# Optimization experiments

Measured on AMD Instinct MI355X. Metric: run time of the kernel, lower is better.

The kernel has to match this reference:

```python
import jax, jax.numpy as jnp
import numpy as np

HEADS = 16
DIM_HEAD = 64


def setup_inputs() -> dict:
    key = jax.random.key(0)
    k1, k2, k3 = jax.random.split(key, 3)
    b, n, dim = 2, 2048, 1024
    x = jax.random.normal(k1, (b, n, dim), dtype=jnp.float32)
    W_qkv = jax.random.normal(k2, (dim, 6 * HEADS * DIM_HEAD), dtype=jnp.float32) * 0.02
    W_out = jax.random.normal(k3, (HEADS * DIM_HEAD, dim), dtype=jnp.float32) * 0.02
    return {"x": x, "W_qkv": W_qkv, "W_out": W_out}


def reference(x, W_qkv, W_out):
    b, n, _ = x.shape
    h, d = HEADS, DIM_HEAD
    scale = d ** -0.5

    # project and split into 6 head-wise tensors: (qkv h d) grouping order
    qkv = (x @ W_qkv).reshape(b, n, 6, h, d).transpose(2, 0, 3, 1, 4)  # [6,b,h,n,d]
    qu, ku, vu, qc, kc, vc = qkv
    qu_s = qu * scale
    qc_s = qc * scale

    idx = jnp.arange(n)
    future = idx[None, :] > idx[:, None]  # torch triu(1): True strictly above diag

    # term1: qc . vu, zeroed on future positions
    term1 = jnp.einsum('bhid,bhjd->bhij', qc_s, vu)
    term1 = jnp.where(future, 0.0, term1)

    # sigmoid lookahead attention, kept ONLY on strictly-future positions
    lookahead = jax.nn.sigmoid(jnp.einsum('bhid,bhjd->bhij', qu_s, ku))
    lookahead = jnp.where(future, lookahead, 0.0)

    # Su[i,k] = sum_j term1[i,j] * lookahead[k,j]
    Su = jnp.einsum('bhij,bhkj->bhik', term1, lookahead)
    Sc = jnp.einsum('bhid,bhjd->bhij', qc_s, kc)

    scores = Sc - jax.nn.silu(Su)
    neg = -jnp.finfo(scores.dtype).max
    scores = jnp.where(future, neg, scores)

    attn = jax.nn.softmax(scores, axis=-1)
    out = jnp.einsum('bhij,bhjd->bhid', attn, vc)  # [b,h,n,d]

    out = out.transpose(0, 2, 1, 3).reshape(b, n, h * d)
    return out @ W_out
```

## Files before the change

### kernel.cpp

```cpp
#include <hip/hip_runtime.h>
#include <hip/hip_bf16.h>
#include <stdint.h>


typedef unsigned short u16;
typedef __attribute__((ext_vector_type(8))) short s8v;
typedef __attribute__((ext_vector_type(4))) float f4v;

__device__ __forceinline__ u16 f2bf(float f) {
  union { float f; unsigned u; } v; v.f = f;
  unsigned r = v.u + 0x7FFFu + ((v.u >> 16) & 1u);
  return (u16)(r >> 16);
}
__device__ __forceinline__ float bf2f(u16 u) {
  union { unsigned u; float f; } v; v.u = ((unsigned)u) << 16; return v.f;
}

typedef __attribute__((address_space(1))) const void* gas_t;
typedef __attribute__((address_space(3))) void* las_t;
__device__ __forceinline__ void gld16(const void* g, void* l) {
  __builtin_amdgcn_global_load_lds((gas_t)g, (las_t)l, 16, 0, 0);
}

__device__ __forceinline__ void zero_acc(f4v acc[4][4]) {
  f4v z = {0.f, 0.f, 0.f, 0.f};
#pragma unroll
  for (int m = 0; m < 4; ++m)
#pragma unroll
    for (int n = 0; n < 4; ++n) acc[m][n] = z;
}


__global__ void convert_x_kernel(const float* __restrict__ in, u16* __restrict__ out) {
  int i = (blockIdx.x * 256 + threadIdx.x) * 4;
  float4 v = *(const float4*)(&in[i]);
  out[i + 0] = f2bf(v.x);
  out[i + 1] = f2bf(v.y);
  out[i + 2] = f2bf(v.z);
  out[i + 3] = f2bf(v.w);
}

__global__ void transpose_convert_kernel(const float* __restrict__ in, u16* __restrict__ out,
                                         int R, int C) {
  __shared__ float tile[32][33];
  int c0 = blockIdx.x * 32, r0 = blockIdx.y * 32;
  for (int rr = threadIdx.y; rr < 32; rr += 8)
    tile[rr][threadIdx.x] = in[(size_t)(r0 + rr) * C + (c0 + threadIdx.x)];
  __syncthreads();
  for (int cc = threadIdx.y; cc < 32; cc += 8)
    out[(size_t)(c0 + cc) * R + (r0 + threadIdx.x)] = f2bf(tile[threadIdx.x][cc]);
}


__global__ __launch_bounds__(256, 2) void gemm_qkv_kernel(
    const u16* __restrict__ xb, const u16* __restrict__ wqkvT,
    u16* __restrict__ quS, u16* __restrict__ ku, u16* __restrict__ vu,
    u16* __restrict__ qcS, u16* __restrict__ kc, u16* __restrict__ vcN) {
  __shared__ u16 sA[2][8192];
  __shared__ u16 sB[2][8192];
  int bm = blockIdx.x, bn = blockIdx.y;
  int tid = threadIdx.x, lane = tid & 63, w = tid >> 6, wm = w >> 1, wn = w & 1;
  int g = lane >> 4, l15 = lane & 15;
  const int sz = (l15 & 7) << 3;
  const int bo = tid * 16;

  const u16* Ab = xb + (size_t)(bm * 128) * 1024;
  const u16* Bb = wqkvT + (size_t)(bn * 128) * 1024;

  auto stg = [&](const u16* base, int ks, u16* dst) {
#pragma unroll
    for (int it = 0; it < 4; ++it) {
      int o = bo + it * 4096;
      int row = o >> 7, lo = o & 127;
      gld16(base + (size_t)row * 1024 + ks * 64 + ((lo ^ ((row & 7) << 4)) >> 1),
            (char*)dst + o);
    }
  };

  f4v acc[4][4];
  zero_acc(acc);
  stg(Ab, 0, sA[0]);
  stg(Bb, 0, sB[0]);
  stg(Ab, 1, sA[1]);
  stg(Bb, 1, sB[1]);

  for (int ks = 0; ks < 16; ++ks) {
    int buf = ks & 1;
    if (ks < 15)
      asm volatile("s_waitcnt vmcnt(8)" ::: "memory");
    else
      asm volatile("s_waitcnt vmcnt(0)" ::: "memory");
    __builtin_amdgcn_sched_barrier(0);
    __builtin_amdgcn_s_barrier();
    __builtin_amdgcn_sched_barrier(0);
#pragma unroll
    for (int kk = 0; kk < 2; ++kk) {
      int c2 = kk * 32 + g * 8;
      s8v a[4], b[4];
#pragma unroll
      for (int m = 0; m < 4; ++m)
        a[m] = *(const s8v*)(&sA[buf][(wm * 64 + m * 16 + l15) * 64 + (c2 ^ sz)]);
#pragma unroll
      for (int n = 0; n < 4; ++n)
        b[n] = *(const s8v*)(&sB[buf][(wn * 64 + n * 16 + l15) * 64 + (c2 ^ sz)]);
#pragma unroll
      for (int m = 0; m < 4; ++m)
#pragma unroll
        for (int n = 0; n < 4; ++n)
          acc[m][n] = __builtin_amdgcn_mfma_f32_16x16x32_bf16(a[m], b[n], acc[m][n], 0, 0, 0);
    }
    __builtin_amdgcn_s_barrier();
    if (ks + 2 < 16) {
      stg(Ab, ks + 2, sA[buf]);
      stg(Bb, ks + 2, sB[buf]);
    }
  }

  int s = bn >> 3;
  int b = bm >> 4;
  int nn0 = (bm & 15) * 128;
  int hh0 = (bn & 7) * 2;
  float scale = (s == 0 || s == 3) ? 0.125f : 1.f;
  u16* obase;
  switch (s) {
    case 0: obase = quS; break;
    case 1: obase = ku; break;
    case 2: obase = vu; break;
    case 3: obase = qcS; break;
    case 4: obase = kc; break;
    default: obase = vcN; break;
  }
  u16* sE = (u16*)sA;
#pragma unroll
  for (int pass = 0; pass < 2; ++pass) {
    __syncthreads();
    if (wn == pass) {
#pragma unroll
      for (int m = 0; m < 4; ++m)
#pragma unroll
        for (int n = 0; n < 4; ++n)
#pragma unroll
          for (int j = 0; j < 4; ++j) {
            int lrow = wm * 64 + m * 16 + g * 4 + j;
            int d = n * 16 + l15;
            sE[lrow * 64 + d] = f2bf(acc[m][n][j] * scale);
          }
    }
    __syncthreads();
    int bh = (b << 4) + hh0 + pass;
    u16* dst = obase + ((size_t)bh * 2048 + nn0) * 64;
    for (int it = 0; it < 4; ++it) {
      int e = (tid + it * 256) * 8;
      *(uint4*)(dst + e) = *(const uint4*)(&sE[e]);
    }
  }
}


__global__ __launch_bounds__(256) void transpose_v_kernel(const u16* __restrict__ vcN,
                                                          u16* __restrict__ vcT) {
  __shared__ u16 t[64][72];
  int nt = blockIdx.x, bh = blockIdx.y;
  const u16* src = vcN + ((size_t)bh * 2048 + nt * 64) * 64;
  int tid = threadIdx.x;
  for (int i = tid; i < 512; i += 256) {
    int r = i >> 3, cseg = i & 7;
    *(uint4*)(&t[r][cseg * 8]) = *(const uint4*)(src + r * 64 + cseg * 8);
  }
  __syncthreads();
  u16* dst = vcT + (size_t)bh * 64 * 2048 + nt * 64;
  for (int i = tid; i < 512; i += 256) {
    int d = i >> 3, nseg = i & 7;
    u16 tmp[8];
#pragma unroll
    for (int e = 0; e < 8; ++e) tmp[e] = t[nseg * 8 + e][d];
    *(uint4*)(dst + (size_t)d * 2048 + nseg * 8) = *(uint4*)tmp;
  }
}


__global__ __launch_bounds__(256, 2) void tl_kernel(
    const u16* __restrict__ qcS, const u16* __restrict__ vu,
    const u16* __restrict__ quS, const u16* __restrict__ ku,
    u16* __restrict__ term1p, u16* __restrict__ lookp, int c0) {
  __shared__ u16 S[32768];
  int t = blockIdx.x, lb = blockIdx.y, bh = c0 + lb;
  int I = 0;
  while ((I + 1) * (I + 2) / 2 <= t) ++I;
  int K = t - I * (I + 1) / 2;
  int tid = threadIdx.x, lane = tid & 63, w = tid >> 6, wm = w >> 1, wn = w & 1;
  int g = lane >> 4, l15 = lane & 15;
  const int sz = (l15 & 7) << 3;
  const int bo = tid * 16;

  auto stg = [&](const u16* base, int rt, u16* dst) {
#pragma unroll
    for (int it = 0; it < 4; ++it) {
      int o = bo + it * 4096;
      int row = o >> 7, lo = o & 127;
      gld16(base + ((size_t)bh * 2048 + rt * 128 + row) * 64 + ((lo ^ ((row & 7) << 4)) >> 1),
            (char*)dst + o);
    }
  };
  stg(qcS, I, S);
  stg(vu, K, S + 8192);
  stg(quS, K, S + 16384);
  stg(ku, I, S + 24576);

  asm volatile("s_waitcnt vmcnt(0)" ::: "memory");
  __builtin_amdgcn_sched_barrier(0);
  __syncthreads();

  f4v acc1[4][4], acc2[4][4];
  zero_acc(acc1);
  zero_acc(acc2);
#pragma unroll
  for (int kk = 0; kk < 2; ++kk) {
    int c2 = kk * 32 + g * 8;
    s8v a1[4], b1[4], a2[4], b2[4];
#pragma unroll
    for (int m = 0; m < 4; ++m) {
      a1[m] = *(const s8v*)(&S[(wm * 64 + m * 16 + l15) * 64 + (c2 ^ sz)]);
      a2[m] = *(const s8v*)(&S[16384 + (wm * 64 + m * 16 + l15) * 64 + (c2 ^ sz)]);
    }
#pragma unroll
    for (int n = 0; n < 4; ++n) {
      b1[n] = *(const s8v*)(&S[8192 + (wn * 64 + n * 16 + l15) * 64 + (c2 ^ sz)]);
      b2[n] = *(const s8v*)(&S[24576 + (wn * 64 + n * 16 + l15) * 64 + (c2 ^ sz)]);
    }
#pragma unroll
    for (int m = 0; m < 4; ++m)
#pragma unroll
      for (int n = 0; n < 4; ++n) {
        acc1[m][n] = __builtin_amdgcn_mfma_f32_16x16x32_bf16(a1[m], b1[n], acc1[m][n], 0, 0, 0);
        acc2[m][n] = __builtin_amdgcn_mfma_f32_16x16x32_bf16(a2[m], b2[n], acc2[m][n], 0, 0, 0);
      }
  }
  __syncthreads();

#pragma unroll
  for (int m = 0; m < 4; ++m)
#pragma unroll
    for (int n = 0; n < 4; ++n)
#pragma unroll
      for (int j4 = 0; j4 < 4; ++j4) {
        int lr = wm * 64 + m * 16 + g * 4 + j4;
        int lc = wn * 64 + n * 16 + l15;
        int idx = wn * 8192 + lr * 64 + ((lc & 63) ^ ((lr & 7) << 3));
        float v1 = acc1[m][n][j4];
        v1 = ((K * 128 + lc) > (I * 128 + lr)) ? 0.f : v1;
        S[idx] = f2bf(v1);
        float v2 = acc2[m][n][j4];
        v2 = ((I * 128 + lc) > (K * 128 + lr)) ? (1.f / (1.f + __expf(-v2))) : 0.f;
        S[16384 + idx] = f2bf(v2);
      }
  __syncthreads();

  u16* o1 = term1p + ((size_t)lb * 136 + t) * 16384;
  u16* o2 = lookp + ((size_t)lb * 136 + t) * 16384;
#pragma unroll
  for (int it = 0; it < 8; ++it) {
    int e = (tid + it * 256) * 8;
    *(uint4*)(o1 + e) = *(const uint4*)(&S[e]);
    *(uint4*)(o2 + e) = *(const uint4*)(&S[16384 + e]);
  }
}


__global__ __launch_bounds__(512, 1) void castle_kernel(
    const u16* __restrict__ term1p, const u16* __restrict__ lookp,
    const u16* __restrict__ qcS, const u16* __restrict__ kc,
    const u16* __restrict__ vcT, const u16* __restrict__ ztile,
    u16* __restrict__ opart, float* __restrict__ ml, int c0) {
  __shared__ u16 S[65536];
  int bid = blockIdx.x;
  int lb = bid / 36, sid = bid % 36;
  int bh = c0 + lb;
  int d = 7, rem = sid;
  while (rem >= 8 - d) { rem -= 8 - d; --d; }
  int Kp = rem, Ip = Kp + d;

  int tid = threadIdx.x, lane = tid & 63, w = tid >> 6;
  int g = lane >> 4, l15 = lane & 15;
  const int sz = (l15 & 7) << 3;
  int rhalf = w >> 2, rsub = w & 3;
  int i_t = 2 * Ip + rhalf;
  int rowbase = rsub * 32;
  const int bo = tid * 16;

  const char* t1b = (const char*)(term1p + (size_t)lb * 136 * 16384);
  const char* lkb = (const char*)(lookp + (size_t)lb * 136 * 16384);

  s8v qa[2][2];
#pragma unroll
  for (int mg = 0; mg < 2; ++mg)
#pragma unroll
    for (int kk = 0; kk < 2; ++kk)
      qa[mg][kk] = *(const s8v*)(&qcS[((size_t)bh * 2048 + i_t * 128 + rowbase + mg * 16 + l15) *
                                          64 + kk * 32 + g * 8]);

  f4v su[2][16];
  {
    f4v z = {0.f, 0.f, 0.f, 0.f};
#pragma unroll
    for (int mg = 0; mg < 2; ++mg)
#pragma unroll
      for (int n = 0; n < 16; ++n) su[mg][n] = z;
  }

  auto stage = [&](int h, int buf) {
    int jt = h >> 1, hf = h & 1;
    const char* a0 = (jt <= 2 * Ip)
                         ? t1b + (size_t)(2 * Ip * (2 * Ip + 1) / 2 + jt) * 32768 + hf * 16384
                         : (const char*)ztile;
    const char* a1 = t1b + (size_t)((2 * Ip + 1) * (2 * Ip + 2) / 2 + jt) * 32768 + hf * 16384;
    const char* b0 = lkb + (size_t)(jt * (jt + 1) / 2 + 2 * Kp) * 32768 + hf * 16384;
    const char* b1 = (jt >= 2 * Kp + 1)
                         ? lkb + (size_t)(jt * (jt + 1) / 2 + 2 * Kp + 1) * 32768 + hf * 16384
                         : (const char*)ztile;
    char* dst = (char*)S + buf * 65536;
#pragma unroll
    for (int r = 0; r < 2; ++r) {
      gld16(a0 + bo + r * 8192, dst + bo + r * 8192);
      gld16(a1 + bo + r * 8192, dst + 16384 + bo + r * 8192);
      gld16(b0 + bo + r * 8192, dst + 32768 + bo + r * 8192);
      gld16(b1 + bo + r * 8192, dst + 49152 + bo + r * 8192);
    }
  };

  const int h0 = 4 * Kp, h1 = 4 * Ip + 3;
  stage(h0, 0);
  for (int h = h0; h <= h1; ++h) {
    int cur = (h - h0) & 1;
    if (h < h1) {
      stage(h + 1, cur ^ 1);
      asm volatile("s_waitcnt vmcnt(8)" ::: "memory");
    } else {
      asm volatile("s_waitcnt vmcnt(0)" ::: "memory");
    }
    __builtin_amdgcn_sched_barrier(0);
    __builtin_amdgcn_s_barrier();
    __builtin_amdgcn_sched_barrier(0);
    const u16* TA = S + cur * 32768 + rhalf * 8192;
    const u16* LB = S + cur * 32768 + 16384;
    __builtin_amdgcn_s_setprio(1);
#pragma unroll
    for (int kk = 0; kk < 2; ++kk) {
      int c2 = kk * 32 + g * 8;
      s8v a[2];
      a[0] = *(const s8v*)(&TA[(rowbase + l15) * 64 + (c2 ^ sz)]);
      a[1] = *(const s8v*)(&TA[(rowbase + 16 + l15) * 64 + (c2 ^ sz)]);
#pragma unroll
      for (int n = 0; n < 16; ++n) {
        s8v b = *(const s8v*)(&LB[(n >> 3) * 8192 + ((n & 7) * 16 + l15) * 64 + (c2 ^ sz)]);
        su[0][n] = __builtin_amdgcn_mfma_f32_16x16x32_bf16(a[0], b, su[0][n], 0, 0, 0);
        su[1][n] = __builtin_amdgcn_mfma_f32_16x16x32_bf16(a[1], b, su[1][n], 0, 0, 0);
      }
    }
    __builtin_amdgcn_s_setprio(0);
    __builtin_amdgcn_s_barrier();
  }

  {
#pragma unroll
    for (int it = 0; it < 4; ++it) {
      int o = bo + it * 8192;
      int row = o >> 7, lo = o & 127;
      const u16* src = kc + ((size_t)bh * 2048 + Kp * 256 + row) * 64 +
                       ((lo ^ ((row & 7) << 4)) >> 1);
      gld16(src, (char*)S + o);
    }
#pragma unroll
    for (int it = 0; it < 4; ++it) {
      int o = bo + it * 8192;
      int kq = o >> 13, oc = o & 8191;
      int dr = oc >> 7, lo = oc & 127;
      const u16* src = vcT + ((size_t)bh * 64 + dr) * 2048 + Kp * 256 + kq * 64 +
                       ((lo ^ ((dr & 7) << 4)) >> 1);
      gld16(src, (char*)S + 32768 + o);
    }
  }
#pragma unroll
  for (int mg = 0; mg < 2; ++mg)
#pragma unroll
    for (int n = 0; n < 16; ++n)
#pragma unroll
      for (int j4 = 0; j4 < 4; ++j4) {
        float xv = su[mg][n][j4];
        su[mg][n][j4] = -(xv / (1.f + __expf(-xv)));
      }
  __syncthreads();

#pragma unroll
  for (int kk = 0; kk < 2; ++kk) {
    int c = kk * 32 + g * 8;
#pragma unroll
    for (int n = 0; n < 16; ++n) {
      s8v b = *(const s8v*)(&S[(n * 16 + l15) * 64 + (c ^ sz)]);
      su[0][n] = __builtin_amdgcn_mfma_f32_16x16x32_bf16(qa[0][kk], b, su[0][n], 0, 0, 0);
      su[1][n] = __builtin_amdgcn_mfma_f32_16x16x32_bf16(qa[1][kk], b, su[1][n], 0, 0, 0);
    }
  }

#pragma unroll
  for (int mg = 0; mg < 2; ++mg)
#pragma unroll
    for (int n = 0; n < 16; ++n)
#pragma unroll
      for (int j4 = 0; j4 < 4; ++j4) {
        int grow = i_t * 128 + rowbase + mg * 16 + g * 4 + j4;
        int gcol = Kp * 256 + n * 16 + l15;
        if (gcol > grow) su[mg][n][j4] = -3.0e38f;
      }

  float mrow[2][4], lrow[2][4];
#pragma unroll
  for (int mg = 0; mg < 2; ++mg)
#pragma unroll
    for (int j4 = 0; j4 < 4; ++j4) {
      float v = -3.0e38f;
#pragma unroll
      for (int n = 0; n < 16; ++n) v = fmaxf(v, su[mg][n][j4]);
      v = fmaxf(v, __shfl_xor(v, 1));
      v = fmaxf(v, __shfl_xor(v, 2));
      v = fmaxf(v, __shfl_xor(v, 4));
      v = fmaxf(v, __shfl_xor(v, 8));
      mrow[mg][j4] = v;
      float sum = 0.f;
#pragma unroll
      for (int n = 0; n < 16; ++n) {
        float e = __expf(su[mg][n][j4] - v);
        su[mg][n][j4] = e;
        sum += e;
      }
      sum += __shfl_xor(sum, 1);
      sum += __shfl_xor(sum, 2);
      sum += __shfl_xor(sum, 4);
      sum += __shfl_xor(sum, 8);
      lrow[mg][j4] = sum;
    }

  f4v o[2][4];
  {
    f4v z = {0.f, 0.f, 0.f, 0.f};
#pragma unroll
    for (int mg = 0; mg < 2; ++mg)
#pragma unroll
      for (int nd = 0; nd < 4; ++nd) o[mg][nd] = z;
  }
  u16* Pw = S + 32768 + w * 2048;
#pragma unroll
  for (int kq = 0; kq < 4; ++kq) {
#pragma unroll
    for (int mg = 0; mg < 2; ++mg)
#pragma unroll
      for (int j4 = 0; j4 < 4; ++j4) {
        int rl = mg * 16 + g * 4 + j4;
        int psz = (rl & 7) << 3;
#pragma unroll
        for (int nn = 0; nn < 4; ++nn) {
          int pc = nn * 16 + l15;
          Pw[rl * 64 + (pc ^ psz)] = f2bf(su[mg][kq * 4 + nn][j4]);
        }
      }
    asm volatile("s_waitcnt lgkmcnt(0)" ::: "memory");
    __builtin_amdgcn_sched_barrier(0);
#pragma unroll
    for (int kk = 0; kk < 2; ++kk) {
      int c = kk * 32 + g * 8;
      s8v pa[2], vb[4];
      pa[0] = *(const s8v*)(&Pw[(l15) * 64 + (c ^ sz)]);
      pa[1] = *(const s8v*)(&Pw[(16 + l15) * 64 + (c ^ sz)]);
#pragma unroll
      for (int nd = 0; nd < 4; ++nd)
        vb[nd] = *(const s8v*)(&S[16384 + kq * 4096 + (nd * 16 + l15) * 64 + (c ^ sz)]);
#pragma unroll
      for (int mg = 0; mg < 2; ++mg)
#pragma unroll
        for (int nd = 0; nd < 4; ++nd)
          o[mg][nd] = __builtin_amdgcn_mfma_f32_16x16x32_bf16(pa[mg], vb[nd], o[mg][nd], 0, 0, 0);
    }
  }

  size_t tb = (size_t)lb * 128 + i_t * 8 + Kp;
#pragma unroll
  for (int mg = 0; mg < 2; ++mg)
#pragma unroll
    for (int nd = 0; nd < 4; ++nd)
#pragma unroll
      for (int j4 = 0; j4 < 4; ++j4) {
        int prow = rowbase + mg * 16 + g * 4 + j4;
        int dcol = nd * 16 + l15;
        opart[(tb * 128 + prow) * 64 + dcol] = f2bf(o[mg][nd][j4]);
      }
  if (l15 == 0) {
#pragma unroll
    for (int mg = 0; mg < 2; ++mg)
#pragma unroll
      for (int j4 = 0; j4 < 4; ++j4) {
        int prow = rowbase + mg * 16 + g * 4 + j4;
        ml[tb * 256 + prow] = mrow[mg][j4];
        ml[tb * 256 + 128 + prow] = lrow[mg][j4];
      }
  }
}


__global__ __launch_bounds__(256) void combine_kernel(const u16* __restrict__ opart,
                                                      const float* __restrict__ ml,
                                                      u16* __restrict__ attn, int c0) {
  int lb = blockIdx.x, I = blockIdx.y, bh = c0 + lb;
  int tid = threadIdx.x;
  int row = tid >> 1, dh = (tid & 1) << 5;
  float M = -3.0e38f, L = 0.f;
  float O[32];
#pragma unroll
  for (int i = 0; i < 32; ++i) O[i] = 0.f;
  int kmax = I >> 1;
  for (int K = 0; K <= kmax; ++K) {
    size_t tb = (size_t)lb * 128 + I * 8 + K;
    float m = ml[tb * 256 + row];
    float l = ml[tb * 256 + 128 + row];
    float newM = fmaxf(M, m);
    float so = __expf(M - newM), sn = __expf(m - newM);
    L = L * so + l * sn;
    const u16* op = opart + (tb * 128 + row) * 64 + dh;
#pragma unroll
    for (int q = 0; q < 4; ++q) {
      s8v ov = *(const s8v*)(op + q * 8);
#pragma unroll
      for (int e = 0; e < 8; ++e)
        O[q * 8 + e] = O[q * 8 + e] * so + bf2f((u16)ov[e]) * sn;
    }
    M = newM;
  }
  float inv = 1.f / L;
  int b = bh >> 4, hh = bh & 15;
  u16* dst = attn + ((size_t)b * 2048 + I * 128 + row) * 1024 + hh * 64 + dh;
#pragma unroll
  for (int i = 0; i < 32; ++i) dst[i] = f2bf(O[i] * inv);
}


__global__ __launch_bounds__(256, 2) void gemm_out_kernel(const u16* __restrict__ attn,
                                                          const u16* __restrict__ woutT,
                                                          float* __restrict__ out) {
  __shared__ u16 sA[2][8192];
  __shared__ u16 sB[2][8192];
  int bm = blockIdx.x, bn = blockIdx.y;
  int tid = threadIdx.x, lane = tid & 63, w = tid >> 6, wm = w >> 1, wn = w & 1;
  int g = lane >> 4, l15 = lane & 15;
  const int sz = (l15 & 7) << 3;
  const int bo = tid * 16;

  const u16* Ab = attn + (size_t)(bm * 128) * 1024;
  const u16* Bb = woutT + (size_t)(bn * 128) * 1024;

  auto stg = [&](const u16* base, int ks, u16* dst) {
#pragma unroll
    for (int it = 0; it < 4; ++it) {
      int o = bo + it * 4096;
      int row = o >> 7, lo = o & 127;
      gld16(base + (size_t)row * 1024 + ks * 64 + ((lo ^ ((row & 7) << 4)) >> 1),
            (char*)dst + o);
    }
  };

  f4v acc[4][4];
  zero_acc(acc);
  stg(Ab, 0, sA[0]);
  stg(Bb, 0, sB[0]);
  stg(Ab, 1, sA[1]);
  stg(Bb, 1, sB[1]);

  for (int ks = 0; ks < 16; ++ks) {
    int buf = ks & 1;
    if (ks < 15)
      asm volatile("s_waitcnt vmcnt(8)" ::: "memory");
    else
      asm volatile("s_waitcnt vmcnt(0)" ::: "memory");
    __builtin_amdgcn_sched_barrier(0);
    __builtin_amdgcn_s_barrier();
    __builtin_amdgcn_sched_barrier(0);
#pragma unroll
    for (int kk = 0; kk < 2; ++kk) {
      int c2 = kk * 32 + g * 8;
      s8v a[4], b[4];
#pragma unroll
      for (int m = 0; m < 4; ++m)
        a[m] = *(const s8v*)(&sA[buf][(wm * 64 + m * 16 + l15) * 64 + (c2 ^ sz)]);
#pragma unroll
      for (int n = 0; n < 4; ++n)
        b[n] = *(const s8v*)(&sB[buf][(wn * 64 + n * 16 + l15) * 64 + (c2 ^ sz)]);
#pragma unroll
      for (int m = 0; m < 4; ++m)
#pragma unroll
        for (int n = 0; n < 4; ++n)
          acc[m][n] = __builtin_amdgcn_mfma_f32_16x16x32_bf16(a[m], b[n], acc[m][n], 0, 0, 0);
    }
    __builtin_amdgcn_s_barrier();
    if (ks + 2 < 16) {
      stg(Ab, ks + 2, sA[buf]);
      stg(Bb, ks + 2, sB[buf]);
    }
  }

#pragma unroll
  for (int m = 0; m < 4; ++m)
#pragma unroll
    for (int n = 0; n < 4; ++n)
#pragma unroll
      for (int j = 0; j < 4; ++j) {
        int row = bm * 128 + wm * 64 + m * 16 + g * 4 + j;
        int col = bn * 128 + wn * 64 + n * 16 + l15;
        out[(size_t)row * 1024 + col] = acc[m][n][j];
      }
}


extern "C" void kernel_launch(void* const* d_in, const int* in_sizes, int n_in,
                              void* d_out, int out_size, void* d_ws, size_t ws_size,
                              hipStream_t stream) {
  const float* x = (const float*)d_in[0];
  const float* Wqkv = (const float*)d_in[1];
  const float* Wout = (const float*)d_in[2];
  float* out = (float*)d_out;

  char* base = (char*)d_ws;
  size_t off = 0;
  auto alloc = [&](size_t bytes) -> void* {
    void* p = base + off;
    off += (bytes + 255) & ~(size_t)255;
    return p;
  };

  u16* woutT = (u16*)alloc(1024ull * 1024 * 2);
  u16* quS = (u16*)alloc(32ull * 2048 * 64 * 2);
  u16* ku = (u16*)alloc(32ull * 2048 * 64 * 2);
  u16* vu = (u16*)alloc(32ull * 2048 * 64 * 2);
  u16* qcS = (u16*)alloc(32ull * 2048 * 64 * 2);
  u16* kc = (u16*)alloc(32ull * 2048 * 64 * 2);
  u16* vcN = (u16*)alloc(32ull * 2048 * 64 * 2);
  u16* vcT = (u16*)alloc(32ull * 2048 * 64 * 2);
  u16* attn = (u16*)alloc(4096ull * 1024 * 2);
  u16* ztile = (u16*)alloc(16384);

  size_t perBH = 136ull * 16384 * 2 * 2 + 128ull * 128 * 64 * 2 + 128ull * 256 * 4;
  size_t remain = (ws_size > off) ? (ws_size - off) : 0;
  int chunk = (int)(remain / perBH);
  if (chunk < 1) chunk = 1;
  if (chunk > 32) chunk = 32;
  u16* term1p = (u16*)alloc((size_t)chunk * 136 * 16384 * 2);
  u16* lookp = (u16*)alloc((size_t)chunk * 136 * 16384 * 2);
  u16* opart = (u16*)alloc((size_t)chunk * 128 * 8192 * 2);
  float* mlb = (float*)alloc((size_t)chunk * 128 * 256 * 4);

  u16* xb;
  u16* wqkvT;
  if ((size_t)chunk * 136 * 16384 * 2 >= (4096ull + 6144ull) * 1024 * 2) {
    xb = term1p;
    wqkvT = term1p + 4096ull * 1024;
  } else {
    xb = (u16*)alloc(4096ull * 1024 * 2);
    wqkvT = (u16*)alloc(6144ull * 1024 * 2);
  }

  hipMemsetAsync(ztile, 0, 16384, stream);
  convert_x_kernel<<<4096, 256, 0, stream>>>(x, xb);
  transpose_convert_kernel<<<dim3(192, 32), dim3(32, 8), 0, stream>>>(Wqkv, wqkvT, 1024, 6144);
  transpose_convert_kernel<<<dim3(32, 32), dim3(32, 8), 0, stream>>>(Wout, woutT, 1024, 1024);
  gemm_qkv_kernel<<<dim3(32, 48), 256, 0, stream>>>(xb, wqkvT, quS, ku, vu, qcS, kc, vcN);
  transpose_v_kernel<<<dim3(32, 32), 256, 0, stream>>>(vcN, vcT);

  for (int c0 = 0; c0 < 32; c0 += chunk) {
    int nb = (32 - c0 < chunk) ? (32 - c0) : chunk;
    tl_kernel<<<dim3(136, nb), 256, 0, stream>>>(qcS, vu, quS, ku, term1p, lookp, c0);
    castle_kernel<<<dim3(36 * nb), 512, 0, stream>>>(term1p, lookp, qcS, kc, vcT, ztile,
                                                     opart, mlb, c0);
    combine_kernel<<<dim3(nb, 16), 256, 0, stream>>>(opart, mlb, attn, c0);
  }
  gemm_out_kernel<<<dim3(32, 8), 256, 0, stream>>>(attn, woutT, out);
}
```

Before: 496.1 us.

## Retile castle kernel warps to 64x128 subtiles and merge column halves in-block

Each of the 8 warps in the castle kernel now computes a 64-row by 128-column sub-tile instead of a 32-row by 256-column strip. This raises the number of MFMAs per LDS fragment load in the Su accumulation loop. The two column-half warps then merge their softmax partials (max, sum, output) through shared memory before writing. The partial-output layout and combine kernel change to match, with 64-row groups and twice as many combine blocks. Register pressure rises from the larger accumulator and qa arrays, and the merge adds two block barriers and an LDS round trip.

```diff
diff --git a/kernel.cpp b/kernel.cpp
--- a/kernel.cpp
+++ b/kernel.cpp
@@ -276,36 +276,28 @@
   int bid = blockIdx.x;
   int lb = bid / 36, sid = bid % 36;
   int bh = c0 + lb;
-  int d = 7, rem = sid;
-  while (rem >= 8 - d) { rem -= 8 - d; --d; }
-  int Kp = rem, Ip = Kp + d;
+  int dd = 7, rem = sid;
+  while (rem >= 8 - dd) { rem -= 8 - dd; --dd; }
+  int Kp = rem, Ip = Kp + dd;
 
   int tid = threadIdx.x, lane = tid & 63, w = tid >> 6;
   int g = lane >> 4, l15 = lane & 15;
   const int sz = (l15 & 7) << 3;
-  int rhalf = w >> 2, rsub = w & 3;
-  int i_t = 2 * Ip + rhalf;
-  int rowbase = rsub * 32;
+  int rp = w >> 1, cp = w & 1;
+  int i_t = 2 * Ip + (rp >> 1);
+  int rowb = (rp & 1) * 64;
   const int bo = tid * 16;
 
   const char* t1b = (const char*)(term1p + (size_t)lb * 136 * 16384);
   const char* lkb = (const char*)(lookp + (size_t)lb * 136 * 16384);
 
-  s8v qa[2][2];
-#pragma unroll
-  for (int mg = 0; mg < 2; ++mg)
-#pragma unroll
-    for (int kk = 0; kk < 2; ++kk)
-      qa[mg][kk] = *(const s8v*)(&qcS[((size_t)bh * 2048 + i_t * 128 + rowbase + mg * 16 + l15) *
-                                          64 + kk * 32 + g * 8]);
-
-  f4v su[2][16];
+  f4v su[4][8];
   {
     f4v z = {0.f, 0.f, 0.f, 0.f};
 #pragma unroll
-    for (int mg = 0; mg < 2; ++mg)
-#pragma unroll
-      for (int n = 0; n < 16; ++n) su[mg][n] = z;
+    for (int mg = 0; mg < 4; ++mg)
+#pragma unroll
+      for (int n = 0; n < 8; ++n) su[mg][n] = z;
   }
 
   auto stage = [&](int h, int buf) {
@@ -341,25 +333,36 @@
     __builtin_amdgcn_sched_barrier(0);
     __builtin_amdgcn_s_barrier();
     __builtin_amdgcn_sched_barrier(0);
-    const u16* TA = S + cur * 32768 + rhalf * 8192;
-    const u16* LB = S + cur * 32768 + 16384;
+    const u16* TA = S + cur * 32768 + (rp >> 1) * 8192;
+    const u16* LB = S + cur * 32768 + 16384 + cp * 8192;
     __builtin_amdgcn_s_setprio(1);
 #pragma unroll
     for (int kk = 0; kk < 2; ++kk) {
       int c2 = kk * 32 + g * 8;
-      s8v a[2];
-      a[0] = *(const s8v*)(&TA[(rowbase + l15) * 64 + (c2 ^ sz)]);
-      a[1] = *(const s8v*)(&TA[(rowbase + 16 + l15) * 64 + (c2 ^ sz)]);
-#pragma unroll
-      for (int n = 0; n < 16; ++n) {
-        s8v b = *(const s8v*)(&LB[(n >> 3) * 8192 + ((n & 7) * 16 + l15) * 64 + (c2 ^ sz)]);
-        su[0][n] = __builtin_amdgcn_mfma_f32_16x16x32_bf16(a[0], b, su[0][n], 0, 0, 0);
-        su[1][n] = __builtin_amdgcn_mfma_f32_16x16x32_bf16(a[1], b, su[1][n], 0, 0, 0);
-      }
+      s8v a[4], b[8];
+#pragma unroll
+      for (int mg = 0; mg < 4; ++mg)
+        a[mg] = *(const s8v*)(&TA[(rowb + mg * 16 + l15) * 64 + (c2 ^ sz)]);
+#pragma unroll
+      for (int n = 0; n < 8; ++n)
+        b[n] = *(const s8v*)(&LB[(n * 16 + l15) * 64 + (c2 ^ sz)]);
+#pragma unroll
+      for (int mg = 0; mg < 4; ++mg)
+#pragma unroll
+        for (int n = 0; n < 8; ++n)
+          su[mg][n] = __builtin_amdgcn_mfma_f32_16x16x32_bf16(a[mg], b[n], su[mg][n], 0, 0, 0);
     }
     __builtin_amdgcn_s_setprio(0);
     __builtin_amdgcn_s_barrier();
   }
+
+  s8v qa[4][2];
+#pragma unroll
+  for (int mg = 0; mg < 4; ++mg)
+#pragma unroll
+    for (int kk = 0; kk < 2; ++kk)
+      qa[mg][kk] = *(const s8v*)(&qcS[((size_t)bh * 2048 + i_t * 128 + rowb + mg * 16 + l15) *
+                                          64 + kk * 32 + g * 8]);
 
   {
 #pragma unroll
@@ -381,9 +384,9 @@
     }
   }
 #pragma unroll
-  for (int mg = 0; mg < 2; ++mg)
-#pragma unroll
-    for (int n = 0; n < 16; ++n)
+  for (int mg = 0; mg < 4; ++mg)
+#pragma unroll
+    for (int n = 0; n < 8; ++n)
 #pragma unroll
       for (int j4 = 0; j4 < 4; ++j4) {
         float xv = su[mg][n][j4];
@@ -395,32 +398,33 @@
   for (int kk = 0; kk < 2; ++kk) {
     int c = kk * 32 + g * 8;
 #pragma unroll
-    for (int n = 0; n < 16; ++n) {
-      s8v b = *(const s8v*)(&S[(n * 16 + l15) * 64 + (c ^ sz)]);
-      su[0][n] = __builtin_amdgcn_mfma_f32_16x16x32_bf16(qa[0][kk], b, su[0][n], 0, 0, 0);
-      su[1][n] = __builtin_amdgcn_mfma_f32_16x16x32_bf16(qa[1][kk], b, su[1][n], 0, 0, 0);
-    }
-  }
-
-#pragma unroll
-  for (int mg = 0; mg < 2; ++mg)
-#pragma unroll
-    for (int n = 0; n < 16; ++n)
+    for (int n = 0; n < 8; ++n) {
+      s8v b = *(const s8v*)(&S[(cp * 128 + n * 16 + l15) * 64 + (c ^ sz)]);
+#pragma unroll
+      for (int mg = 0; mg < 4; ++mg)
+        su[mg][n] = __builtin_amdgcn_mfma_f32_16x16x32_bf16(qa[mg][kk], b, su[mg][n], 0, 0, 0);
+    }
+  }
+
+#pragma unroll
+  for (int mg = 0; mg < 4; ++mg)
+#pragma unroll
+    for (int n = 0; n < 8; ++n)
 #pragma unroll
       for (int j4 = 0; j4 < 4; ++j4) {
-        int grow = i_t * 128 + rowbase + mg * 16 + g * 4 + j4;
-        int gcol = Kp * 256 + n * 16 + l15;
+        int grow = i_t * 128 + rowb + mg * 16 + g * 4 + j4;
+        int gcol = Kp * 256 + cp * 128 + n * 16 + l15;
         if (gcol > grow) su[mg][n][j4] = -3.0e38f;
       }
 
-  float mrow[2][4], lrow[2][4];
-#pragma unroll
-  for (int mg = 0; mg < 2; ++mg)
+  float mrow[4][4], lrow[4][4];
+#pragma unroll
+  for (int mg = 0; mg < 4; ++mg)
 #pragma unroll
     for (int j4 = 0; j4 < 4; ++j4) {
       float v = -3.0e38f;
 #pragma unroll
-      for (int n = 0; n < 16; ++n) v = fmaxf(v, su[mg][n][j4]);
+      for (int n = 0; n < 8; ++n) v = fmaxf(v, su[mg][n][j4]);
       v = fmaxf(v, __shfl_xor(v, 1));
       v = fmaxf(v, __shfl_xor(v, 2));
       v = fmaxf(v, __shfl_xor(v, 4));
@@ -428,7 +432,7 @@
       mrow[mg][j4] = v;
       float sum = 0.f;
 #pragma unroll
-      for (int n = 0; n < 16; ++n) {
+      for (int n = 0; n < 8; ++n) {
         float e = __expf(su[mg][n][j4] - v);
         su[mg][n][j4] = e;
         sum += e;
@@ -440,27 +444,22 @@
       lrow[mg][j4] = sum;
     }
 
-  f4v o[2][4];
-  {
-    f4v z = {0.f, 0.f, 0.f, 0.f};
-#pragma unroll
-    for (int mg = 0; mg < 2; ++mg)
-#pragma unroll
-      for (int nd = 0; nd < 4; ++nd) o[mg][nd] = z;
-  }
-  u16* Pw = S + 32768 + w * 2048;
-#pragma unroll
-  for (int kq = 0; kq < 4; ++kq) {
-#pragma unroll
-    for (int mg = 0; mg < 2; ++mg)
+  f4v o[4][4];
+  zero_acc(o);
+  u16* Pw = S + 32768 + w * 4096;
+#pragma unroll
+  for (int kq2 = 0; kq2 < 2; ++kq2) {
+    int kq = cp * 2 + kq2;
+#pragma unroll
+    for (int mg = 0; mg < 4; ++mg)
 #pragma unroll
       for (int j4 = 0; j4 < 4; ++j4) {
         int rl = mg * 16 + g * 4 + j4;
-        int psz = (rl & 7) << 3;
+        int psz = ((g * 4 + j4) & 7) << 3;
 #pragma unroll
         for (int nn = 0; nn < 4; ++nn) {
           int pc = nn * 16 + l15;
-          Pw[rl * 64 + (pc ^ psz)] = f2bf(su[mg][kq * 4 + nn][j4]);
+          Pw[rl * 64 + (pc ^ psz)] = f2bf(su[mg][kq2 * 4 + nn][j4]);
         }
       }
     asm volatile("s_waitcnt lgkmcnt(0)" ::: "memory");
@@ -468,39 +467,62 @@
 #pragma unroll
     for (int kk = 0; kk < 2; ++kk) {
       int c = kk * 32 + g * 8;
-      s8v pa[2], vb[4];
-      pa[0] = *(const s8v*)(&Pw[(l15) * 64 + (c ^ sz)]);
-      pa[1] = *(const s8v*)(&Pw[(16 + l15) * 64 + (c ^ sz)]);
+      s8v pa[4], vb[4];
+#pragma unroll
+      for (int mg = 0; mg < 4; ++mg)
+        pa[mg] = *(const s8v*)(&Pw[(mg * 16 + l15) * 64 + (c ^ sz)]);
 #pragma unroll
       for (int nd = 0; nd < 4; ++nd)
         vb[nd] = *(const s8v*)(&S[16384 + kq * 4096 + (nd * 16 + l15) * 64 + (c ^ sz)]);
 #pragma unroll
-      for (int mg = 0; mg < 2; ++mg)
+      for (int mg = 0; mg < 4; ++mg)
 #pragma unroll
         for (int nd = 0; nd < 4; ++nd)
           o[mg][nd] = __builtin_amdgcn_mfma_f32_16x16x32_bf16(pa[mg], vb[nd], o[mg][nd], 0, 0, 0);
     }
   }
 
-  size_t tb = (size_t)lb * 128 + i_t * 8 + Kp;
-#pragma unroll
-  for (int mg = 0; mg < 2; ++mg)
-#pragma unroll
-    for (int nd = 0; nd < 4; ++nd)
+  __syncthreads();
+  if (cp == 1) {
+    float* Od = (float*)S + rp * 4096;
+    float* Ml = (float*)((char*)S + 65536) + rp * 128;
+#pragma unroll
+    for (int mg = 0; mg < 4; ++mg)
 #pragma unroll
       for (int j4 = 0; j4 < 4; ++j4) {
-        int prow = rowbase + mg * 16 + g * 4 + j4;
-        int dcol = nd * 16 + l15;
-        opart[(tb * 128 + prow) * 64 + dcol] = f2bf(o[mg][nd][j4]);
-      }
-  if (l15 == 0) {
-#pragma unroll
-    for (int mg = 0; mg < 2; ++mg)
+        int row = mg * 16 + g * 4 + j4;
+#pragma unroll
+        for (int nd = 0; nd < 4; ++nd) Od[row * 64 + nd * 16 + l15] = o[mg][nd][j4];
+        if (l15 == 0) {
+          Ml[row] = mrow[mg][j4];
+          Ml[64 + row] = lrow[mg][j4];
+        }
+      }
+  }
+  __syncthreads();
+  if (cp == 0) {
+    float* Od = (float*)S + rp * 4096;
+    float* Ml = (float*)((char*)S + 65536) + rp * 128;
+    size_t tb = ((size_t)lb * 32 + i_t * 2 + (rp & 1)) * 8 + Kp;
+#pragma unroll
+    for (int mg = 0; mg < 4; ++mg)
 #pragma unroll
       for (int j4 = 0; j4 < 4; ++j4) {
-        int prow = rowbase + mg * 16 + g * 4 + j4;
-        ml[tb * 256 + prow] = mrow[mg][j4];
-        ml[tb * 256 + 128 + prow] = lrow[mg][j4];
+        int row = mg * 16 + g * 4 + j4;
+        float m1 = Ml[row], l1 = Ml[64 + row];
+        float m0 = mrow[mg][j4], l0 = lrow[mg][j4];
+        float nm = fmaxf(m0, m1);
+        float s0 = __expf(m0 - nm), s1 = __expf(m1 - nm);
+        if (l15 == 0) {
+          ml[tb * 128 + row] = nm;
+          ml[tb * 128 + 64 + row] = l0 * s0 + l1 * s1;
+        }
+#pragma unroll
+        for (int nd = 0; nd < 4; ++nd) {
+          int dcol = nd * 16 + l15;
+          float val = o[mg][nd][j4] * s0 + Od[row * 64 + dcol] * s1;
+          opart[(tb * 64 + row) * 64 + dcol] = f2bf(val);
+        }
       }
   }
 }
@@ -509,36 +531,38 @@
 __global__ __launch_bounds__(256) void combine_kernel(const u16* __restrict__ opart,
                                                       const float* __restrict__ ml,
                                                       u16* __restrict__ attn, int c0) {
-  int lb = blockIdx.x, I = blockIdx.y, bh = c0 + lb;
+  int lb = blockIdx.x, rg = blockIdx.y, bh = c0 + lb;
+  int i_t = rg >> 1;
   int tid = threadIdx.x;
-  int row = tid >> 1, dh = (tid & 1) << 5;
+  int row = tid >> 2, dh = (tid & 3) << 4;
   float M = -3.0e38f, L = 0.f;
-  float O[32];
-#pragma unroll
-  for (int i = 0; i < 32; ++i) O[i] = 0.f;
-  int kmax = I >> 1;
-  for (int K = 0; K <= kmax; ++K) {
-    size_t tb = (size_t)lb * 128 + I * 8 + K;
-    float m = ml[tb * 256 + row];
-    float l = ml[tb * 256 + 128 + row];
-    float newM = fmaxf(M, m);
-    float so = __expf(M - newM), sn = __expf(m - newM);
+  float O[16];
+#pragma unroll
+  for (int i = 0; i < 16; ++i) O[i] = 0.f;
+  int np = (i_t >> 1) + 1;
+  for (int Kp = 0; Kp < np; ++Kp) {
+    size_t tb = ((size_t)lb * 32 + rg) * 8 + Kp;
+    float m = ml[tb * 128 + row];
+    float l = ml[tb * 128 + 64 + row];
+    float nM = fmaxf(M, m);
+    float so = __expf(M - nM), sn = __expf(m - nM);
     L = L * so + l * sn;
-    const u16* op = opart + (tb * 128 + row) * 64 + dh;
-#pragma unroll
-    for (int q = 0; q < 4; ++q) {
+    const u16* op = opart + (tb * 64 + row) * 64 + dh;
+#pragma unroll
+    for (int q = 0; q < 2; ++q) {
       s8v ov = *(const s8v*)(op + q * 8);
 #pragma unroll
       for (int e = 0; e < 8; ++e)
         O[q * 8 + e] = O[q * 8 + e] * so + bf2f((u16)ov[e]) * sn;
     }
-    M = newM;
+    M = nM;
   }
   float inv = 1.f / L;
   int b = bh >> 4, hh = bh & 15;
-  u16* dst = attn + ((size_t)b * 2048 + I * 128 + row) * 1024 + hh * 64 + dh;
-#pragma unroll
-  for (int i = 0; i < 32; ++i) dst[i] = f2bf(O[i] * inv);
+  int grow = i_t * 128 + (rg & 1) * 64 + row;
+  u16* dst = attn + ((size_t)b * 2048 + grow) * 1024 + hh * 64 + dh;
+#pragma unroll
+  for (int i = 0; i < 16; ++i) dst[i] = f2bf(O[i] * inv);
 }
 
 
@@ -645,15 +669,15 @@
   u16* attn = (u16*)alloc(4096ull * 1024 * 2);
   u16* ztile = (u16*)alloc(16384);
 
-  size_t perBH = 136ull * 16384 * 2 * 2 + 128ull * 128 * 64 * 2 + 128ull * 256 * 4;
+  size_t perBH = 136ull * 16384 * 2 * 2 + 256ull * 4096 * 2 + 256ull * 128 * 4;
   size_t remain = (ws_size > off) ? (ws_size - off) : 0;
   int chunk = (int)(remain / perBH);
   if (chunk < 1) chunk = 1;
   if (chunk > 32) chunk = 32;
   u16* term1p = (u16*)alloc((size_t)chunk * 136 * 16384 * 2);
   u16* lookp = (u16*)alloc((size_t)chunk * 136 * 16384 * 2);
-  u16* opart = (u16*)alloc((size_t)chunk * 128 * 8192 * 2);
-  float* mlb = (float*)alloc((size_t)chunk * 128 * 256 * 4);
+  u16* opart = (u16*)alloc((size_t)chunk * 256 * 4096 * 2);
+  float* mlb = (float*)alloc((size_t)chunk * 256 * 128 * 4);
 
   u16* xb;
   u16* wqkvT;
@@ -677,7 +701,7 @@
     tl_kernel<<<dim3(136, nb), 256, 0, stream>>>(qcS, vu, quS, ku, term1p, lookp, c0);
     castle_kernel<<<dim3(36 * nb), 512, 0, stream>>>(term1p, lookp, qcS, kc, vcT, ztile,
                                                      opart, mlb, c0);
-    combine_kernel<<<dim3(nb, 16), 256, 0, stream>>>(opart, mlb, attn, c0);
+    combine_kernel<<<dim3(nb, 32), 256, 0, stream>>>(opart, mlb, attn, c0);
   }
   gemm_out_kernel<<<dim3(32, 8), 256, 0, stream>>>(attn, woutT, out);
 }
```

Result: slower. 590.5 us (+19.0%).
